# Kernel tuning notes

Measured on AMD Instinct MI355X. Metric: run time of the kernel, lower is better.

Reference implementation:

```python
import jax, jax.numpy as jnp
import numpy as np

B = 4096          # batch_size * world_size
D = 256           # embedding dim
TEMP = 0.5        # temperature
EPS = 1e-8        # torch CosineSimilarity eps


def setup_inputs() -> dict:
    key = jax.random.key(0)
    k1, k2 = jax.random.split(key)
    z_i = jax.random.normal(k1, (B, D), dtype=jnp.float32)
    z_j = jax.random.normal(k2, (B, D), dtype=jnp.float32)
    return {"z_i": z_i, "z_j": z_j}


def reference(z_i, z_j):
    N = 2 * B
    z = jnp.concatenate([z_i, z_j], axis=0)                      # [N, D]
    # Cosine similarity: normalize rows (clamped norm like torch eps), then matmul.
    norms = jnp.maximum(jnp.linalg.norm(z, axis=1, keepdims=True), EPS)
    zn = z / norms
    sim = jnp.matmul(zn, zn.T) / TEMP                            # [N, N]
    # Positive pairs: offsets +B and -B from the diagonal.
    pos = jnp.concatenate([jnp.diagonal(sim, B), jnp.diagonal(sim, -B)])  # [N]
    # Cross-entropy with label 0 over [pos, negatives]:
    # logsumexp over {pos} U {negatives} == logsumexp over row excluding the diagonal
    # (the (i, i±B) entries removed by the mask are exactly re-added as the positive).
    neg_inf = jnp.array(-jnp.inf, dtype=sim.dtype)
    sim_nodiag = jnp.where(jnp.eye(N, dtype=bool), neg_inf, sim)
    lse = jax.nn.logsumexp(sim_nodiag, axis=1)                   # [N]
    loss = jnp.sum(lse - pos) / N                                # reduction='sum' then /N
    return loss
```

## Files before the change

kernel.cpp:

```cpp
#include <hip/hip_runtime.h>

#define NROWS 8192
#define DIM   256
#define BHALF 4096
#define NCHUNK 8
#define SQRT2 1.41421356237f

typedef unsigned char u8;
typedef __attribute__((ext_vector_type(4))) float f32x4;
typedef __attribute__((ext_vector_type(4))) int   i32x4;
typedef __attribute__((ext_vector_type(8))) int   i32x8;

__device__ inline void gload_lds16(const void* g, void* l) {
  __builtin_amdgcn_global_load_lds(
      (const __attribute__((address_space(1))) void*)g,
      (__attribute__((address_space(3))) void*)l, 16, 0, 0);
}

__global__ __launch_bounds__(256) void nrm_kernel(const float* __restrict__ zi,
                                                  const float* __restrict__ zj,
                                                  u8* __restrict__ zn8,
                                                  float* __restrict__ out) {
  if (blockIdx.x == 0 && threadIdx.x == 0) out[0] = 0.f;
  const int w = threadIdx.x >> 6, l = threadIdx.x & 63;
  const int row = blockIdx.x * 4 + w;
  const float* src = (row < BHALF) ? zi + (size_t)row * DIM
                                   : zj + (size_t)(row - BHALF) * DIM;
  float4 v = *(const float4*)(src + l * 4);
  float ss = v.x * v.x + v.y * v.y + v.z * v.z + v.w * v.w;
#pragma unroll
  for (int m = 1; m < 64; m <<= 1) ss += __shfl_xor(ss, m);
  float inv = SQRT2 / fmaxf(sqrtf(ss), 1e-8f);
  int p = __builtin_amdgcn_cvt_pk_fp8_f32(v.x * inv, v.y * inv, 0, false);
  p = __builtin_amdgcn_cvt_pk_fp8_f32(v.z * inv, v.w * inv, p, true);
  *(int*)(zn8 + (size_t)row * DIM + (size_t)l * 4) = p;
}

__global__ __launch_bounds__(256, 2) void sim_kernel(const u8* __restrict__ zn8,
                                                     float* __restrict__ partials,
                                                     float* __restrict__ pos) {
  __shared__ __align__(16) u8 Bsm[2][128 * DIM];
  __shared__ float plane[2][128];

  const int t = threadIdx.x;
  const int w = t >> 6, l = t & 63;
  const int wa = w >> 1, wb = w & 1;
  const int rl = l & 15, kg = l >> 4;

  const int rp = (int)blockIdx.x >> 3;
  const int ch = (int)blockIdx.x & 7;
  const int colbase = ch * 1024;

  auto STAGE = [&](int base_row, u8* dst) {
#pragma unroll
    for (int i = 0; i < 8; ++i) {
      int c = i * 256 + t;
      int r = c >> 4, cd = c & 15;
      int cs = (cd & 8) | ((cd ^ r) & 7);
      gload_lds16(zn8 + (size_t)(base_row + r) * DIM + (size_t)cs * 16,
                  dst + (size_t)((i * 256 + w * 64) * 16));
    }
  };
  auto RD = [&](const u8* buf, int row, int k) -> i32x8 {
    const int salt = row & 7;
    i32x4 lo = *(const i32x4*)(buf + row * DIM + ((k * 8 + ((kg * 2) ^ salt)) << 4));
    i32x4 hi = *(const i32x4*)(buf + row * DIM + ((k * 8 + ((kg * 2 + 1) ^ salt)) << 4));
    return __builtin_shufflevector(lo, hi, 0, 1, 2, 3, 4, 5, 6, 7);
  };

  STAGE(rp * 128, &Bsm[0][0]);
  STAGE(colbase, &Bsm[1][0]);
  asm volatile("s_waitcnt vmcnt(8)" ::: "memory");
  __builtin_amdgcn_sched_barrier(0);
  __builtin_amdgcn_s_barrier();
  __builtin_amdgcn_sched_barrier(0);

  i32x8 pb[4][2];
#pragma unroll
  for (int pj = 0; pj < 4; ++pj)
#pragma unroll
    for (int k = 0; k < 2; ++k)
      pb[pj][k] = RD(&Bsm[0][0], wb * 64 + pj * 16 + rl, k);
  asm volatile("s_waitcnt lgkmcnt(0)" ::: "memory");
  __builtin_amdgcn_sched_barrier(0);
  __builtin_amdgcn_s_barrier();
  __builtin_amdgcn_sched_barrier(0);
  STAGE(colbase + 128, &Bsm[0][0]);

  const int dtile = ((rp >> 3) == ch) ? (rp & 7) : -1;
  const int pg = (rp < 32) ? (rp + 32) : (rp - 32);
  const int ptile = ((pg >> 3) == ch) ? (pg & 7) : -1;

  float rsum[4] = {0.f, 0.f, 0.f, 0.f};
  float pv[4]   = {0.f, 0.f, 0.f, 0.f};

#pragma unroll 2
  for (int ti = 0; ti < 8; ++ti) {
    if (ti < 7) asm volatile("s_waitcnt vmcnt(8)" ::: "memory");
    else        asm volatile("s_waitcnt vmcnt(0)" ::: "memory");
    __builtin_amdgcn_sched_barrier(0);
    __builtin_amdgcn_s_barrier();
    __builtin_amdgcn_sched_barrier(0);

    u8* Bb = &Bsm[(ti & 1) ^ 1][0];

    i32x8 af[4][2];
#pragma unroll
    for (int ci = 0; ci < 4; ++ci)
#pragma unroll
      for (int k = 0; k < 2; ++k)
        af[ci][k] = RD(Bb, wa * 64 + ci * 16 + rl, k);
    asm volatile("s_waitcnt lgkmcnt(0)" ::: "memory");
    __builtin_amdgcn_sched_barrier(0);
    __builtin_amdgcn_s_barrier();
    __builtin_amdgcn_sched_barrier(0);
    if (ti < 6) STAGE(colbase + (ti + 2) * 128, Bb);

    f32x4 acc[4][4];
#pragma unroll
    for (int i = 0; i < 4; ++i)
#pragma unroll
      for (int j = 0; j < 4; ++j) acc[i][j] = (f32x4){0.f, 0.f, 0.f, 0.f};

#pragma unroll
    for (int k = 0; k < 2; ++k)
#pragma unroll
      for (int ci = 0; ci < 4; ++ci)
#pragma unroll
        for (int pj = 0; pj < 4; ++pj)
          acc[ci][pj] = __builtin_amdgcn_mfma_scale_f32_16x16x128_f8f6f4(
              af[ci][k], pb[pj][k], acc[ci][pj],
              0, 0,
              0, 0x7f7f7f7f,
              0, 0x7f7f7f7f);

    if (ti == dtile) {
#pragma unroll
      for (int ci = 0; ci < 4; ++ci)
#pragma unroll
        for (int pj = 0; pj < 4; ++pj)
#pragma unroll
          for (int jj = 0; jj < 4; ++jj) {
            float e = __expf(acc[ci][pj][jj]);
            bool skip = (wa == wb) && (ci == pj) && (kg == (rl >> 2)) && (jj == (rl & 3));
            rsum[pj] += skip ? 0.f : e;
          }
    } else {
#pragma unroll
      for (int ci = 0; ci < 4; ++ci)
#pragma unroll
        for (int pj = 0; pj < 4; ++pj)
#pragma unroll
          for (int jj = 0; jj < 4; ++jj)
            rsum[pj] += __expf(acc[ci][pj][jj]);
    }
    if (ti == ptile && wa == wb && kg == (rl >> 2)) {
#pragma unroll
      for (int ci = 0; ci < 4; ++ci) pv[ci] = acc[ci][ci][rl & 3];
    }
  }

#pragma unroll
  for (int pj = 0; pj < 4; ++pj) {
    rsum[pj] += __shfl_xor(rsum[pj], 16);
    rsum[pj] += __shfl_xor(rsum[pj], 32);
  }
  if (kg == 0) {
#pragma unroll
    for (int pj = 0; pj < 4; ++pj)
      plane[wa][wb * 64 + pj * 16 + rl] = rsum[pj];
  }
  __syncthreads();
  if (t < 128)
    partials[(size_t)ch * NROWS + rp * 128 + t] = plane[0][t] + plane[1][t];
  if (ptile >= 0 && wa == wb && kg == (rl >> 2)) {
#pragma unroll
    for (int ci = 0; ci < 4; ++ci)
      pos[rp * 128 + wb * 64 + ci * 16 + rl] = pv[ci];
  }
}

__global__ __launch_bounds__(256) void fin_kernel(const float* __restrict__ partials,
                                                  const float* __restrict__ pos,
                                                  float* __restrict__ out) {
  const int r = blockIdx.x * 256 + threadIdx.x;
  float s = 0.f;
#pragma unroll
  for (int ch = 0; ch < NCHUNK; ++ch) s += partials[(size_t)ch * NROWS + r];
  float v = logf(s) - pos[r];
#pragma unroll
  for (int m = 1; m < 64; m <<= 1) v += __shfl_xor(v, m);
  __shared__ float wsum[4];
  const int w = threadIdx.x >> 6, l = threadIdx.x & 63;
  if (l == 0) wsum[w] = v;
  __syncthreads();
  if (threadIdx.x == 0)
    atomicAdd(out, (wsum[0] + wsum[1] + wsum[2] + wsum[3]) * (1.f / NROWS));
}

extern "C" void kernel_launch(void* const* d_in, const int* in_sizes, int n_in,
                              void* d_out, int out_size, void* d_ws, size_t ws_size,
                              hipStream_t stream) {
  const float* zi = (const float*)d_in[0];
  const float* zj = (const float*)d_in[1];

  u8*    zn8      = (u8*)d_ws;
  float* partials = (float*)((char*)d_ws + (size_t)NROWS * DIM);
  float* pos      = (float*)((char*)partials + (size_t)NCHUNK * NROWS * 4);
  float* out      = (float*)d_out;

  nrm_kernel<<<NROWS / 4, 256, 0, stream>>>(zi, zj, zn8, out);
  sim_kernel<<<64 * NCHUNK, 256, 0, stream>>>(zn8, partials, pos);
  fin_kernel<<<NROWS / 256, 256, 0, stream>>>(partials, pos, out);
}
```

Measured before the change: 32.59 us.

## Fold log2e into normalization scale and pipeline LDS reads with per-row-block MFMA

The normalization scale changes from sqrt(2) to sqrt(2*log2 e), so the similarity comes out in base-2 units. That lets the kernel use the hardware exp2 instead of expf, and the positive value is multiplied back by ln2 when stored. The sim loop now single-barrier double-buffers B tiles, issuing the next tile's stage right after the barrier. It software-pipelines A-fragment LDS reads one 16-row block ahead with partial lgkmcnt waits, which cuts the accumulator register footprint from 16 to 4 vectors. MFMA bursts are wrapped in setprio, and the diagonal is handled by subtracting its exp term rather than masking every element, which adds a small rounding difference for that entry.

```diff
diff --git a/kernel.cpp b/kernel.cpp
--- a/kernel.cpp
+++ b/kernel.cpp
@@ -4,7 +4,8 @@
 #define DIM   256
 #define BHALF 4096
 #define NCHUNK 8
-#define SQRT2 1.41421356237f
+#define SCALE 1.69864358f
+#define LN2F  0.69314718f
 
 typedef unsigned char u8;
 typedef __attribute__((ext_vector_type(4))) float f32x4;
@@ -30,7 +31,7 @@
   float ss = v.x * v.x + v.y * v.y + v.z * v.z + v.w * v.w;
 #pragma unroll
   for (int m = 1; m < 64; m <<= 1) ss += __shfl_xor(ss, m);
-  float inv = SQRT2 / fmaxf(sqrtf(ss), 1e-8f);
+  float inv = SCALE / fmaxf(sqrtf(ss), 1e-8f);
   int p = __builtin_amdgcn_cvt_pk_fp8_f32(v.x * inv, v.y * inv, 0, false);
   p = __builtin_amdgcn_cvt_pk_fp8_f32(v.z * inv, v.w * inv, p, true);
   *(int*)(zn8 + (size_t)row * DIM + (size_t)l * 4) = p;
@@ -61,11 +62,15 @@
                   dst + (size_t)((i * 256 + w * 64) * 16));
     }
   };
-  auto RD = [&](const u8* buf, int row, int k) -> i32x8 {
+  auto RD2 = [&](const u8* buf, int row, i32x8* dst) {
     const int salt = row & 7;
-    i32x4 lo = *(const i32x4*)(buf + row * DIM + ((k * 8 + ((kg * 2) ^ salt)) << 4));
-    i32x4 hi = *(const i32x4*)(buf + row * DIM + ((k * 8 + ((kg * 2 + 1) ^ salt)) << 4));
-    return __builtin_shufflevector(lo, hi, 0, 1, 2, 3, 4, 5, 6, 7);
+    const u8* base = buf + row * DIM;
+#pragma unroll
+    for (int k = 0; k < 2; ++k) {
+      i32x4 lo = *(const i32x4*)(base + ((k * 8 + ((kg * 2) ^ salt)) << 4));
+      i32x4 hi = *(const i32x4*)(base + ((k * 8 + ((kg * 2 + 1) ^ salt)) << 4));
+      dst[k] = __builtin_shufflevector(lo, hi, 0, 1, 2, 3, 4, 5, 6, 7);
+    }
   };
 
   STAGE(rp * 128, &Bsm[0][0]);
@@ -78,14 +83,9 @@
   i32x8 pb[4][2];
 #pragma unroll
   for (int pj = 0; pj < 4; ++pj)
-#pragma unroll
-    for (int k = 0; k < 2; ++k)
-      pb[pj][k] = RD(&Bsm[0][0], wb * 64 + pj * 16 + rl, k);
+    RD2(&Bsm[0][0], wb * 64 + pj * 16 + rl, pb[pj]);
   asm volatile("s_waitcnt lgkmcnt(0)" ::: "memory");
   __builtin_amdgcn_sched_barrier(0);
-  __builtin_amdgcn_s_barrier();
-  __builtin_amdgcn_sched_barrier(0);
-  STAGE(colbase + 128, &Bsm[0][0]);
 
   const int dtile = ((rp >> 3) == ch) ? (rp & 7) : -1;
   const int pg = (rp < 32) ? (rp + 32) : (rp - 32);
@@ -93,70 +93,52 @@
 
   float rsum[4] = {0.f, 0.f, 0.f, 0.f};
   float pv[4]   = {0.f, 0.f, 0.f, 0.f};
+  const bool dlane = (wa == wb) && (kg == (rl >> 2));
 
 #pragma unroll 2
   for (int ti = 0; ti < 8; ++ti) {
-    if (ti < 7) asm volatile("s_waitcnt vmcnt(8)" ::: "memory");
-    else        asm volatile("s_waitcnt vmcnt(0)" ::: "memory");
+    asm volatile("s_waitcnt vmcnt(0)" ::: "memory");
     __builtin_amdgcn_sched_barrier(0);
     __builtin_amdgcn_s_barrier();
     __builtin_amdgcn_sched_barrier(0);
 
-    u8* Bb = &Bsm[(ti & 1) ^ 1][0];
+    const u8* Bb = &Bsm[(ti + 1) & 1][0];
+    if (ti < 7) STAGE(colbase + (ti + 1) * 128, &Bsm[ti & 1][0]);
 
-    i32x8 af[4][2];
+    const bool tdiag = (ti == dtile), tpos = (ti == ptile);
+
+    i32x8 af[2][2];
+    RD2(Bb, wa * 64 + rl, af[0]);
 #pragma unroll
-    for (int ci = 0; ci < 4; ++ci)
+    for (int ci = 0; ci < 4; ++ci) {
+      if (ci < 3) RD2(Bb, wa * 64 + (ci + 1) * 16 + rl, af[(ci + 1) & 1]);
+      if (ci < 3) asm volatile("s_waitcnt lgkmcnt(4)" ::: "memory");
+      else        asm volatile("s_waitcnt lgkmcnt(0)" ::: "memory");
+      __builtin_amdgcn_sched_barrier(0);
+
+      f32x4 acc[4];
+#pragma unroll
+      for (int pj = 0; pj < 4; ++pj) acc[pj] = (f32x4){0.f, 0.f, 0.f, 0.f};
+      __builtin_amdgcn_s_setprio(1);
 #pragma unroll
       for (int k = 0; k < 2; ++k)
-        af[ci][k] = RD(Bb, wa * 64 + ci * 16 + rl, k);
-    asm volatile("s_waitcnt lgkmcnt(0)" ::: "memory");
-    __builtin_amdgcn_sched_barrier(0);
-    __builtin_amdgcn_s_barrier();
-    __builtin_amdgcn_sched_barrier(0);
-    if (ti < 6) STAGE(colbase + (ti + 2) * 128, Bb);
-
-    f32x4 acc[4][4];
-#pragma unroll
-    for (int i = 0; i < 4; ++i)
-#pragma unroll
-      for (int j = 0; j < 4; ++j) acc[i][j] = (f32x4){0.f, 0.f, 0.f, 0.f};
-
-#pragma unroll
-    for (int k = 0; k < 2; ++k)
-#pragma unroll
-      for (int ci = 0; ci < 4; ++ci)
 #pragma unroll
         for (int pj = 0; pj < 4; ++pj)
-          acc[ci][pj] = __builtin_amdgcn_mfma_scale_f32_16x16x128_f8f6f4(
-              af[ci][k], pb[pj][k], acc[ci][pj],
+          acc[pj] = __builtin_amdgcn_mfma_scale_f32_16x16x128_f8f6f4(
+              af[ci & 1][k], pb[pj][k], acc[pj],
               0, 0,
               0, 0x7f7f7f7f,
               0, 0x7f7f7f7f);
+      __builtin_amdgcn_s_setprio(0);
 
-    if (ti == dtile) {
 #pragma unroll
-      for (int ci = 0; ci < 4; ++ci)
+      for (int pj = 0; pj < 4; ++pj)
 #pragma unroll
-        for (int pj = 0; pj < 4; ++pj)
-#pragma unroll
-          for (int jj = 0; jj < 4; ++jj) {
-            float e = __expf(acc[ci][pj][jj]);
-            bool skip = (wa == wb) && (ci == pj) && (kg == (rl >> 2)) && (jj == (rl & 3));
-            rsum[pj] += skip ? 0.f : e;
-          }
-    } else {
-#pragma unroll
-      for (int ci = 0; ci < 4; ++ci)
-#pragma unroll
-        for (int pj = 0; pj < 4; ++pj)
-#pragma unroll
-          for (int jj = 0; jj < 4; ++jj)
-            rsum[pj] += __expf(acc[ci][pj][jj]);
-    }
-    if (ti == ptile && wa == wb && kg == (rl >> 2)) {
-#pragma unroll
-      for (int ci = 0; ci < 4; ++ci) pv[ci] = acc[ci][ci][rl & 3];
+        for (int jj = 0; jj < 4; ++jj)
+          rsum[pj] += __builtin_amdgcn_exp2f(acc[pj][jj]);
+      if (tdiag && dlane)
+        rsum[ci] -= __builtin_amdgcn_exp2f(acc[ci][rl & 3]);
+      if (tpos && dlane) pv[ci] = acc[ci][rl & 3];
     }
   }
 
@@ -173,10 +155,10 @@
   __syncthreads();
   if (t < 128)
     partials[(size_t)ch * NROWS + rp * 128 + t] = plane[0][t] + plane[1][t];
-  if (ptile >= 0 && wa == wb && kg == (rl >> 2)) {
+  if (ptile >= 0 && dlane) {
 #pragma unroll
     for (int ci = 0; ci < 4; ++ci)
-      pos[rp * 128 + wb * 64 + ci * 16 + rl] = pv[ci];
+      pos[rp * 128 + wb * 64 + ci * 16 + rl] = pv[ci] * LN2F;
   }
 }
 
```

Result: no change. 32.27 us (-1.0%).
